# Optimization experiments

Hardware: AMD Instinct MI355X
Metric: run time of the kernel (lower is better)

The kernel has to match this reference:

```python
import jax, jax.numpy as jnp
import numpy as np

N_NODES = 50000
N_EDGES = 600000
N_GRAPHS = 512
DIM = 128
N_FEAT = 78
N_LAYERS = 4
BN_EPS = 1e-5


def setup_inputs() -> dict:
    key = jax.random.key(0)
    ks = jax.random.split(key, 12)
    w = lambda k, s: (jax.random.normal(k, s, jnp.float32) * 0.05)
    x = jax.random.normal(ks[0], (N_NODES, N_FEAT), jnp.float32)
    edge_index = jax.random.randint(ks[1], (2, N_EDGES), 0, N_NODES)
    batch = jnp.sort(jax.random.randint(ks[2], (N_NODES,), 0, N_GRAPHS))
    return {
        "x": x,
        "edge_index": edge_index,
        "batch": batch,
        "ini_w1": w(ks[3], (N_FEAT, DIM)),
        "ini_b1": jnp.zeros((DIM,), jnp.float32),
        "ini_w2": w(ks[4], (DIM, DIM)),
        "ini_b2": jnp.zeros((DIM,), jnp.float32),
        "gin_w1": w(ks[5], (N_LAYERS, DIM, DIM)),
        "gin_b1": jnp.zeros((N_LAYERS, DIM), jnp.float32),
        "gin_w2": w(ks[6], (N_LAYERS, DIM, DIM)),
        "gin_b2": jnp.zeros((N_LAYERS, DIM), jnp.float32),
        "bn_gamma": jnp.ones((N_LAYERS, DIM), jnp.float32),
        "bn_beta": jnp.zeros((N_LAYERS, DIM), jnp.float32),
        "layer_w": w(ks[7], (N_LAYERS,)),  # Conv2d(L,1,(1,1)) weight
        "layer_b": jnp.zeros((1,), jnp.float32),
    }


def reference(x, edge_index, batch, ini_w1, ini_b1, ini_w2, ini_b2,
              gin_w1, gin_b1, gin_w2, gin_b2, bn_gamma, bn_beta,
              layer_w, layer_b):
    # ini_embed: Linear -> ReLU -> Linear
    h = jnp.maximum(x @ ini_w1 + ini_b1, 0.0) @ ini_w2 + ini_b2  # [N, D]
    src, dst = edge_index[0], edge_index[1]
    embeds = []
    for i in range(N_LAYERS):
        # GINConv (eps=0): mlp(x_i + sum_{j->i} x_j)
        agg = jax.ops.segment_sum(h[src], dst, num_segments=N_NODES)
        z = h + agg
        z = jnp.maximum(z @ gin_w1[i] + gin_b1[i], 0.0) @ gin_w2[i] + gin_b2[i]
        z = jnp.maximum(z, 0.0)  # F.relu after conv
        # BatchNorm1d (training mode: batch stats, biased var)
        mean = jnp.mean(z, axis=0)
        var = jnp.mean((z - mean) ** 2, axis=0)
        h = (z - mean) * jax.lax.rsqrt(var + BN_EPS) * bn_gamma[i] + bn_beta[i]
        embeds.append(h)
    layer_nodes = jnp.stack(embeds, axis=1)  # [N, L, D]
    # layer_conv Conv2d(L,1,(1,1)): learned weighted sum over layer axis + bias
    pos_global_node = jnp.einsum('nld,l->nd', layer_nodes, layer_w) + layer_b
    # global_add_pool over graphs
    pos_global_graph = jax.ops.segment_sum(pos_global_node, batch,
                                           num_segments=N_GRAPHS)  # [G, D]
    return pos_global_graph
```

## Files before the change

kernel.cpp:

```cpp
#include <hip/hip_runtime.h>

#define N_NODES  50000
#define N_EDGES  600000
#define N_GRAPHS 512
#define DIM      128
#define N_FEAT   78
#define N_LAYERS 4
#define BN_EPS   1e-5f
#define SLOT_CAP 64
#define LDA      136
#define NPART    16

#define NBKT     196
#define NBLK_BIN 128
#define BCAP     64
#define EDGES_PER_BIN ((N_EDGES + NBLK_BIN - 1) / NBLK_BIN)

#define GSTART_BLOCKS 196
#define ZERO_BLOCKS 512
#define GBLOCKS ((N_NODES + 63) / 64)
#define TW_ELEMS (10 * 16384)
#define BN_FLOATS (N_LAYERS * NPART * 256)

typedef __attribute__((ext_vector_type(8))) _Float16 f16x8;
typedef __attribute__((ext_vector_type(4))) float f32x4;

static __device__ __forceinline__ short f2h(float f) {
    _Float16 h = (_Float16)f;
    union { _Float16 h; short s; } u; u.h = h;
    return u.s;
}
static __device__ __forceinline__ float h2f(ushort s) {
    union { ushort s; _Float16 h; } u; u.s = s;
    return (float)u.h;
}


__global__ __launch_bounds__(256) void transpose_weights(const float* __restrict__ ini_w1,
                                                         const float* __restrict__ ini_w2,
                                                         const float* __restrict__ gw1,
                                                         const float* __restrict__ gw2,
                                                         short* __restrict__ wt,
                                                         float* __restrict__ bnstat) {
    int gid = blockIdx.x * 256 + threadIdx.x;
    if (gid < TW_ELEMS) {
        int m = gid >> 14;
        int idx = gid & 16383;
        int n = idx >> 7;
        int k = idx & 127;
        const float* src;
        int K = 128;
        if (m == 0) { src = ini_w1; K = N_FEAT; }
        else if (m == 1) src = ini_w2;
        else if (m < 6) src = gw1 + (m - 2) * 16384;
        else src = gw2 + (m - 6) * 16384;
        float v = (k < K) ? src[k * 128 + n] : 0.f;
        wt[m * 16384 + n * 128 + k] = f2h(v);
    } else {
        int bi = gid - TW_ELEMS;
        if (bi < BN_FLOATS) bnstat[bi] = 0.0f;
    }
}


__global__ __launch_bounds__(256, 4) void ini_fused(const float* __restrict__ x,
                                                    const short* __restrict__ Wt1,
                                                    const float* __restrict__ b1,
                                                    const short* __restrict__ Wt2,
                                                    const float* __restrict__ b2,
                                                    ushort* __restrict__ Cout,
                                                    const int* __restrict__ src,
                                                    const int* __restrict__ dst,
                                                    const int* __restrict__ batch,
                                                    int* __restrict__ bcnt,
                                                    uint* __restrict__ bpool,
                                                    int* __restrict__ gstart,
                                                    float* __restrict__ gsum,
                                                    float* __restrict__ gssq) {
    __shared__ short As[64 * LDA];
    __shared__ short Bs[64 * LDA];
    int tid = threadIdx.x;

    if (blockIdx.x >= GBLOCKS) {
        int b = blockIdx.x - GBLOCKS;
        if (b < NBLK_BIN) {
            int* lcur = (int*)As;
            for (int i = tid; i < NBKT; i += 256) lcur[i] = 0;
            __syncthreads();
            int base = b * EDGES_PER_BIN;
            int lim = min(base + EDGES_PER_BIN, N_EDGES);
            for (int e = base + tid; e < lim; e += 256) {
                int d = dst[e];
                int s = src[e];
                int bk = d >> 8;
                int p = atomicAdd(&lcur[bk], 1);
                if (p < BCAP)
                    bpool[(bk * NBLK_BIN + b) * BCAP + p] =
                        ((uint)(d & 255) << 16) | (uint)s;
            }
            __syncthreads();
            for (int i = tid; i < NBKT; i += 256) bcnt[b * NBKT + i] = lcur[i];
            return;
        }
        b -= NBLK_BIN;
        if (b < GSTART_BLOCKS) {
            int n = b * 256 + tid;
            if (n < N_NODES) {
                int g = batch[n];
                int gp = (n == 0) ? -1 : batch[n - 1];
                for (int gg = gp + 1; gg <= g; ++gg) gstart[gg] = n;
                if (n == N_NODES - 1)
                    for (int gg = g + 1; gg <= N_GRAPHS; ++gg) gstart[gg] = N_NODES;
            }
            return;
        }
        b -= GSTART_BLOCKS;
        float4 z = make_float4(0.f, 0.f, 0.f, 0.f);
        float* bse = (b < 256) ? gsum : gssq;
        int off = (b & 255) * 1024 + tid * 4;
        *(float4*)&bse[off] = z;
        return;
    }

    int row0 = blockIdx.x * 64;
    int wave = tid >> 6;
    int wlane = tid & 63;
    int rw = wave >> 1;
    int cw = wave & 1;
    int lm = wlane & 15;
    int quad = wlane >> 4;
    const int wrow = (cw * 64 + lm) * 128 + quad * 8;

    f16x8 bcur[4], bnxt[4];
    #pragma unroll
    for (int nt = 0; nt < 4; ++nt)
        bcur[nt] = *(const f16x8*)&Wt1[wrow + nt * 2048];

    #pragma unroll
    for (int j = 0; j < 32; ++j) {
        int lin = tid + j * 256;
        int r = lin >> 7;
        int k = lin & 127;
        int gr = row0 + r;
        float v = 0.f;
        if (gr < N_NODES && k < N_FEAT) v = x[gr * N_FEAT + k];
        As[r * LDA + k] = f2h(v);
    }
    __syncthreads();

    f32x4 acc[2][4];
    #pragma unroll
    for (int mt = 0; mt < 2; ++mt)
        #pragma unroll
        for (int nt = 0; nt < 4; ++nt)
            acc[mt][nt] = (f32x4){0.f, 0.f, 0.f, 0.f};

    #pragma unroll
    for (int ks = 0; ks < 4; ++ks) {
        if (ks < 3) {
            #pragma unroll
            for (int nt = 0; nt < 4; ++nt)
                bnxt[nt] = *(const f16x8*)&Wt1[wrow + nt * 2048 + (ks + 1) * 32];
        }
        int kb = ks * 32 + quad * 8;
        f16x8 a0 = *(const f16x8*)&As[(rw * 32 + lm) * LDA + kb];
        f16x8 a1 = *(const f16x8*)&As[(rw * 32 + 16 + lm) * LDA + kb];
        #pragma unroll
        for (int nt = 0; nt < 4; ++nt) {
            acc[0][nt] = __builtin_amdgcn_mfma_f32_16x16x32_f16(a0, bcur[nt], acc[0][nt], 0, 0, 0);
            acc[1][nt] = __builtin_amdgcn_mfma_f32_16x16x32_f16(a1, bcur[nt], acc[1][nt], 0, 0, 0);
        }
        #pragma unroll
        for (int nt = 0; nt < 4; ++nt) bcur[nt] = bnxt[nt];
    }

    #pragma unroll
    for (int nt = 0; nt < 4; ++nt) {
        int col = cw * 64 + nt * 16 + lm;
        float bv = b1[col];
        #pragma unroll
        for (int mt = 0; mt < 2; ++mt) {
            #pragma unroll
            for (int r = 0; r < 4; ++r) {
                int row = rw * 32 + mt * 16 + quad * 4 + r;
                Bs[row * LDA + col] = (short)f2h(fmaxf(acc[mt][nt][r] + bv, 0.f));
            }
        }
    }
    #pragma unroll
    for (int nt = 0; nt < 4; ++nt)
        bcur[nt] = *(const f16x8*)&Wt2[wrow + nt * 2048];
    __syncthreads();

    #pragma unroll
    for (int mt = 0; mt < 2; ++mt)
        #pragma unroll
        for (int nt = 0; nt < 4; ++nt)
            acc[mt][nt] = (f32x4){0.f, 0.f, 0.f, 0.f};
    #pragma unroll
    for (int ks = 0; ks < 4; ++ks) {
        if (ks < 3) {
            #pragma unroll
            for (int nt = 0; nt < 4; ++nt)
                bnxt[nt] = *(const f16x8*)&Wt2[wrow + nt * 2048 + (ks + 1) * 32];
        }
        int kb = ks * 32 + quad * 8;
        f16x8 a0 = *(const f16x8*)&Bs[(rw * 32 + lm) * LDA + kb];
        f16x8 a1 = *(const f16x8*)&Bs[(rw * 32 + 16 + lm) * LDA + kb];
        #pragma unroll
        for (int nt = 0; nt < 4; ++nt) {
            acc[0][nt] = __builtin_amdgcn_mfma_f32_16x16x32_f16(a0, bcur[nt], acc[0][nt], 0, 0, 0);
            acc[1][nt] = __builtin_amdgcn_mfma_f32_16x16x32_f16(a1, bcur[nt], acc[1][nt], 0, 0, 0);
        }
        #pragma unroll
        for (int nt = 0; nt < 4; ++nt) bcur[nt] = bnxt[nt];
    }

    ushort* Cs = (ushort*)As;
    #pragma unroll
    for (int nt = 0; nt < 4; ++nt) {
        int col = cw * 64 + nt * 16 + lm;
        float bv = b2[col];
        #pragma unroll
        for (int mt = 0; mt < 2; ++mt) {
            #pragma unroll
            for (int r = 0; r < 4; ++r) {
                int row = rw * 32 + mt * 16 + quad * 4 + r;
                Cs[row * LDA + col] = (ushort)f2h(acc[mt][nt][r] + bv);
            }
        }
    }
    __syncthreads();

    #pragma unroll
    for (int j = 0; j < 4; ++j) {
        int lin = tid + j * 256;
        int r = lin >> 4;
        int kc = lin & 15;
        int gr = row0 + r;
        if (gr < N_NODES)
            *(uint4*)&Cout[gr * 128 + kc * 8] = *(const uint4*)&Cs[r * LDA + kc * 8];
    }
}


__global__ __launch_bounds__(256) void build_slot(const uint* __restrict__ bpool,
                                                  const int* __restrict__ bcnt,
                                                  int* __restrict__ cnt,
                                                  ushort* __restrict__ slot) {
    __shared__ ushort lslot[256 * SLOT_CAP];
    __shared__ int lcnt[256];
    __shared__ int rcnt[NBLK_BIN];
    int tid = threadIdx.x;
    int bkt = blockIdx.x;
    lcnt[tid] = 0;
    if (tid < NBLK_BIN) rcnt[tid] = min(bcnt[tid * NBKT + bkt], BCAP);
    __syncthreads();
    const uint* pool = bpool + (size_t)bkt * NBLK_BIN * BCAP;
    #pragma unroll 1
    for (int i = tid; i < NBLK_BIN * BCAP; i += 256) {
        int run = i >> 6;
        int pos = i & (BCAP - 1);
        if (pos < rcnt[run]) {
            uint u = pool[i];
            int ls = u >> 16;
            int p = atomicAdd(&lcnt[ls], 1);
            if (p < SLOT_CAP) lslot[ls * SLOT_CAP + p] = (ushort)(u & 0xffffu);
        }
    }
    __syncthreads();
    int node0 = bkt << 8;
    int gn = node0 + tid;
    if (gn < N_NODES) cnt[gn] = lcnt[tid];
    #pragma unroll
    for (int j = 0; j < 8; ++j) {
        int i = tid + j * 256;
        int r = i >> 3;
        int c = i & 7;
        int g = node0 + r;
        if (g < N_NODES)
            *(uint4*)&slot[g * SLOT_CAP + c * 8] = *(const uint4*)&lslot[r * SLOT_CAP + c * 8];
    }
}


__global__ __launch_bounds__(256) void aggregate_h(const ushort* __restrict__ Z,
                                                   const int* __restrict__ cnt,
                                                   const ushort* __restrict__ slot,
                                                   const float* __restrict__ bnpart,
                                                   const float* __restrict__ gamma,
                                                   const float* __restrict__ beta,
                                                   ushort* __restrict__ A) {
    __shared__ float saff[128], taff[128];
    int tid = threadIdx.x;
    if (tid < 128) {
        float s = 1.0f, t = 0.0f;
        if (bnpart) {
            float sum = 0.f, ssq = 0.f;
            #pragma unroll
            for (int p = 0; p < NPART; ++p) {
                sum += bnpart[p * 256 + tid];
                ssq += bnpart[p * 256 + 128 + tid];
            }
            const float invN = 1.0f / (float)N_NODES;
            float m = sum * invN;
            float var = ssq * invN - m * m;
            s = gamma[tid] * rsqrtf(var + BN_EPS);
            t = beta[tid] - m * s;
        }
        saff[tid] = s; taff[tid] = t;
    }
    __syncthreads();

    int node = blockIdx.x * 16 + (tid >> 4);
    if (node >= N_NODES) return;
    int lane = tid & 15;
    float sc[8], tc[8];
    #pragma unroll
    for (int j = 0; j < 8; ++j) {
        sc[j] = saff[lane * 8 + j];
        tc[j] = taff[lane * 8 + j];
    }
    union U { uint4 u; _Float16 h[8]; };
    union I { uint4 u; ushort s[8]; };
    const uint4* z4 = (const uint4*)Z;
    U zu; zu.u = z4[node * 16 + lane];
    float v[8];
    #pragma unroll
    for (int j = 0; j < 8; ++j) v[j] = (float)zu.h[j];
    int dtrue = cnt[node];
    int d = min(dtrue, SLOT_CAP);
    const ushort* sl = slot + node * SLOT_CAP;
    int e = 0;
    for (; e + 8 <= d; e += 8) {
        I si; si.u = *(const uint4*)&sl[e];
        U u[8];
        #pragma unroll
        for (int q = 0; q < 8; ++q) u[q].u = z4[(int)si.s[q] * 16 + lane];
        #pragma unroll
        for (int j = 0; j < 8; ++j) {
            float a = ((float)u[0].h[j] + (float)u[1].h[j]) +
                      ((float)u[2].h[j] + (float)u[3].h[j]);
            float b = ((float)u[4].h[j] + (float)u[5].h[j]) +
                      ((float)u[6].h[j] + (float)u[7].h[j]);
            v[j] += a + b;
        }
    }
    if (e + 4 <= d) {
        int s0 = sl[e], s1 = sl[e + 1], s2 = sl[e + 2], s3 = sl[e + 3];
        U u0, u1, u2, u3;
        u0.u = z4[s0 * 16 + lane];
        u1.u = z4[s1 * 16 + lane];
        u2.u = z4[s2 * 16 + lane];
        u3.u = z4[s3 * 16 + lane];
        #pragma unroll
        for (int j = 0; j < 8; ++j)
            v[j] += ((float)u0.h[j] + (float)u1.h[j]) +
                    ((float)u2.h[j] + (float)u3.h[j]);
        e += 4;
    }
    for (; e < d; ++e) {
        U u; u.u = z4[(int)sl[e] * 16 + lane];
        #pragma unroll
        for (int j = 0; j < 8; ++j) v[j] += (float)u.h[j];
    }
    float dsc = 1.0f + (float)dtrue;
    U ou;
    #pragma unroll
    for (int j = 0; j < 8; ++j)
        ou.h[j] = (_Float16)(sc[j] * v[j] + dsc * tc[j]);
    ((uint4*)A)[node * 16 + lane] = ou.u;
}


__global__ __launch_bounds__(256, 4) void gemm_gin(const ushort* __restrict__ A,
                                                   const short* __restrict__ Wt1,
                                                   const float* __restrict__ b1,
                                                   const short* __restrict__ Wt2,
                                                   const float* __restrict__ b2,
                                                   ushort* __restrict__ C,
                                                   const int* __restrict__ batch,
                                                   float* __restrict__ gsum,
                                                   float* __restrict__ gssq,
                                                   float* __restrict__ bnpart) {
    __shared__ short Bs[64 * LDA];
    __shared__ float scr[256];
    __shared__ int sb[64];
    int tid = threadIdx.x;
    int row0 = blockIdx.x * 64;

    int wave = tid >> 6;
    int wlane = tid & 63;
    int rw = wave >> 1;
    int cw = wave & 1;
    int lm = wlane & 15;
    int quad = wlane >> 4;
    const int wrow = (cw * 64 + lm) * 128 + quad * 8;

    if (tid < 64) {
        int n = row0 + tid;
        sb[tid] = (n < N_NODES) ? batch[n] : -1;
    }

    int r0 = min(row0 + rw * 32 + lm, N_NODES - 1);
    int r1 = min(row0 + rw * 32 + 16 + lm, N_NODES - 1);
    const ushort* arow0 = A + r0 * 128 + quad * 8;
    const ushort* arow1 = A + r1 * 128 + quad * 8;

    f16x8 bcur[4], bnxt[4];
    #pragma unroll
    for (int nt = 0; nt < 4; ++nt)
        bcur[nt] = *(const f16x8*)&Wt1[wrow + nt * 2048];

    f32x4 acc[2][4];
    #pragma unroll
    for (int mt = 0; mt < 2; ++mt)
        #pragma unroll
        for (int nt = 0; nt < 4; ++nt)
            acc[mt][nt] = (f32x4){0.f, 0.f, 0.f, 0.f};

    f16x8 a0 = *(const f16x8*)arow0;
    f16x8 a1 = *(const f16x8*)arow1;
    #pragma unroll
    for (int ks = 0; ks < 4; ++ks) {
        f16x8 a0n, a1n;
        if (ks < 3) {
            a0n = *(const f16x8*)(arow0 + (ks + 1) * 32);
            a1n = *(const f16x8*)(arow1 + (ks + 1) * 32);
            #pragma unroll
            for (int nt = 0; nt < 4; ++nt)
                bnxt[nt] = *(const f16x8*)&Wt1[wrow + nt * 2048 + (ks + 1) * 32];
        }
        #pragma unroll
        for (int nt = 0; nt < 4; ++nt) {
            acc[0][nt] = __builtin_amdgcn_mfma_f32_16x16x32_f16(a0, bcur[nt], acc[0][nt], 0, 0, 0);
            acc[1][nt] = __builtin_amdgcn_mfma_f32_16x16x32_f16(a1, bcur[nt], acc[1][nt], 0, 0, 0);
        }
        a0 = a0n; a1 = a1n;
        #pragma unroll
        for (int nt = 0; nt < 4; ++nt) bcur[nt] = bnxt[nt];
    }

    #pragma unroll
    for (int nt = 0; nt < 4; ++nt) {
        int col = cw * 64 + nt * 16 + lm;
        float bv = b1[col];
        #pragma unroll
        for (int mt = 0; mt < 2; ++mt) {
            #pragma unroll
            for (int r = 0; r < 4; ++r) {
                int row = rw * 32 + mt * 16 + quad * 4 + r;
                Bs[row * LDA + col] = (short)f2h(fmaxf(acc[mt][nt][r] + bv, 0.f));
            }
        }
    }
    #pragma unroll
    for (int nt = 0; nt < 4; ++nt)
        bcur[nt] = *(const f16x8*)&Wt2[wrow + nt * 2048];
    __syncthreads();

    #pragma unroll
    for (int mt = 0; mt < 2; ++mt)
        #pragma unroll
        for (int nt = 0; nt < 4; ++nt)
            acc[mt][nt] = (f32x4){0.f, 0.f, 0.f, 0.f};
    #pragma unroll
    for (int ks = 0; ks < 4; ++ks) {
        if (ks < 3) {
            #pragma unroll
            for (int nt = 0; nt < 4; ++nt)
                bnxt[nt] = *(const f16x8*)&Wt2[wrow + nt * 2048 + (ks + 1) * 32];
        }
        int kb = ks * 32 + quad * 8;
        f16x8 c0 = *(const f16x8*)&Bs[(rw * 32 + lm) * LDA + kb];
        f16x8 c1 = *(const f16x8*)&Bs[(rw * 32 + 16 + lm) * LDA + kb];
        #pragma unroll
        for (int nt = 0; nt < 4; ++nt) {
            acc[0][nt] = __builtin_amdgcn_mfma_f32_16x16x32_f16(c0, bcur[nt], acc[0][nt], 0, 0, 0);
            acc[1][nt] = __builtin_amdgcn_mfma_f32_16x16x32_f16(c1, bcur[nt], acc[1][nt], 0, 0, 0);
        }
        #pragma unroll
        for (int nt = 0; nt < 4; ++nt) bcur[nt] = bnxt[nt];
    }
    __syncthreads();

    ushort* Cs = (ushort*)Bs;
    #pragma unroll
    for (int nt = 0; nt < 4; ++nt) {
        int col = cw * 64 + nt * 16 + lm;
        float bv = b2[col];
        #pragma unroll
        for (int mt = 0; mt < 2; ++mt) {
            #pragma unroll
            for (int r = 0; r < 4; ++r) {
                int row = rw * 32 + mt * 16 + quad * 4 + r;
                Cs[row * LDA + col] = (ushort)f2h(fmaxf(acc[mt][nt][r] + bv, 0.f));
            }
        }
    }
    __syncthreads();

    #pragma unroll
    for (int j = 0; j < 4; ++j) {
        int lin = tid + j * 256;
        int r = lin >> 4;
        int kc = lin & 15;
        int gr = row0 + r;
        if (gr < N_NODES)
            *(uint4*)&C[gr * 128 + kc * 8] = *(const uint4*)&Cs[r * LDA + kc * 8];
    }

    {
        int c = tid & 127;
        int rbase = (tid >> 7) * 32;
        int curg = sb[rbase];
        float rs = 0.f, rss = 0.f;
        float ts = 0.f, tss = 0.f;
        for (int r = rbase; r < rbase + 32; ++r) {
            int g = sb[r];
            if (g < 0) break;
            if (g != curg) {
                atomicAdd(&gsum[curg * 128 + c], rs);
                atomicAdd(&gssq[curg * 128 + c], rss);
                rs = 0.f; rss = 0.f; curg = g;
            }
            float v = h2f(Cs[r * LDA + c]);
            rs += v; rss += v * v;
            ts += v; tss += v * v;
        }
        if (curg >= 0) {
            atomicAdd(&gsum[curg * 128 + c], rs);
            atomicAdd(&gssq[curg * 128 + c], rss);
        }
        if (tid >= 128) { scr[c] = ts; scr[128 + c] = tss; }
        __syncthreads();
        if (tid < 128) {
            float* part = bnpart + (blockIdx.x & (NPART - 1)) * 256;
            atomicAdd(&part[c], ts + scr[c]);
            atomicAdd(&part[128 + c], tss + scr[128 + c]);
        }
    }
}


__global__ __launch_bounds__(256) void combine(const float* __restrict__ gsum,
                                               const float* __restrict__ bnstat,
                                               const int* __restrict__ gstart,
                                               const float* __restrict__ gamma,
                                               const float* __restrict__ beta,
                                               const float* __restrict__ LW,
                                               const float* __restrict__ LB,
                                               float* __restrict__ out) {
    int gid = blockIdx.x * 256 + threadIdx.x;
    if (gid >= N_GRAPHS * 128) return;
    int g = gid >> 7;
    int d = gid & 127;
    float c = (float)(gstart[g + 1] - gstart[g]);
    float o = c * LB[0];
    const float invN = 1.0f / (float)N_NODES;
    #pragma unroll
    for (int l = 0; l < N_LAYERS; ++l) {
        const float* part = bnstat + l * NPART * 256;
        float sum = 0.f, ssq = 0.f;
        #pragma unroll
        for (int p = 0; p < NPART; ++p) {
            sum += part[p * 256 + d];
            ssq += part[p * 256 + 128 + d];
        }
        float m = sum * invN;
        float var = ssq * invN - m * m;
        float s = gamma[l * 128 + d] * rsqrtf(var + BN_EPS);
        float t = beta[l * 128 + d] - m * s;
        o += LW[l] * (s * gsum[(l * N_GRAPHS + g) * 128 + d] + c * t);
    }
    out[gid] = o;
}


extern "C" void kernel_launch(void* const* d_in, const int* in_sizes, int n_in,
                              void* d_out, int out_size, void* d_ws, size_t ws_size,
                              hipStream_t stream) {
    const float* x      = (const float*)d_in[0];
    const int*   ei     = (const int*)d_in[1];
    const int*   batch  = (const int*)d_in[2];
    const float* ini_w1 = (const float*)d_in[3];
    const float* ini_b1 = (const float*)d_in[4];
    const float* ini_w2 = (const float*)d_in[5];
    const float* ini_b2 = (const float*)d_in[6];
    const float* gw1    = (const float*)d_in[7];
    const float* gb1    = (const float*)d_in[8];
    const float* gw2    = (const float*)d_in[9];
    const float* gb2    = (const float*)d_in[10];
    const float* gamma  = (const float*)d_in[11];
    const float* beta   = (const float*)d_in[12];
    const float* lw     = (const float*)d_in[13];
    const float* lb     = (const float*)d_in[14];
    float* out = (float*)d_out;

    char* p = (char*)d_ws;
    auto carve = [&](size_t bytes) -> char* {
        char* q = p;
        p += (bytes + 255) & ~(size_t)255;
        return q;
    };
    ushort* z0    = (ushort*)carve(sizeof(ushort) * N_NODES * DIM);
    ushort* z1    = (ushort*)carve(sizeof(ushort) * N_NODES * DIM);
    ushort* abuf  = (ushort*)carve(sizeof(ushort) * N_NODES * DIM);
    float* bnstat = (float*)carve(sizeof(float) * BN_FLOATS);
    float* gsum   = (float*)carve(sizeof(float) * N_LAYERS * N_GRAPHS * DIM);
    float* gssq   = (float*)carve(sizeof(float) * N_LAYERS * N_GRAPHS * DIM);
    short* wbf    = (short*)carve(sizeof(short) * 10 * 128 * 128);
    int* gstart   = (int*)carve(sizeof(int) * (N_GRAPHS + 1));
    int* cnt      = (int*)carve(sizeof(int) * N_NODES);
    ushort* slot  = (ushort*)carve(sizeof(ushort) * N_NODES * SLOT_CAP);
    int* bcnt     = (int*)carve(sizeof(int) * NBLK_BIN * NBKT);
    uint* bpool   = (uint*)abuf;

    const int* src = ei;
    const int* dst = ei + N_EDGES;

    int twblocks = (TW_ELEMS + BN_FLOATS + 255) / 256;
    transpose_weights<<<twblocks, 256, 0, stream>>>(
        ini_w1, ini_w2, gw1, gw2, wbf, bnstat);

    ini_fused<<<GBLOCKS + NBLK_BIN + GSTART_BLOCKS + ZERO_BLOCKS, 256, 0, stream>>>(
        x, wbf, ini_b1, wbf + 16384, ini_b2, z0,
        src, dst, batch, bcnt, bpool, gstart, gsum, gssq);

    build_slot<<<NBKT, 256, 0, stream>>>(bpool, bcnt, cnt, slot);

    ushort* zprev = z0;
    ushort* znext = z1;
    for (int i = 0; i < N_LAYERS; ++i) {
        const float* bp_in = (i == 0) ? nullptr : bnstat + (i - 1) * NPART * 256;
        const float* gptr  = (i == 0) ? gamma : gamma + (i - 1) * DIM;
        const float* bptr  = (i == 0) ? beta : beta + (i - 1) * DIM;
        aggregate_h<<<(N_NODES + 15) / 16, 256, 0, stream>>>(
            zprev, cnt, slot, bp_in, gptr, bptr, abuf);
        gemm_gin<<<GBLOCKS, 256, 0, stream>>>(
            abuf, wbf + (2 + i) * 16384, gb1 + i * DIM,
            wbf + (6 + i) * 16384, gb2 + i * DIM, znext, batch,
            gsum + i * N_GRAPHS * DIM, gssq + i * N_GRAPHS * DIM,
            bnstat + i * NPART * 256);
        ushort* tmp = zprev; zprev = znext; znext = tmp;
    }
    combine<<<(N_GRAPHS * 128 + 255) / 256, 256, 0, stream>>>(
        gsum, bnstat, gstart, gamma, beta, lw, lb, out);
}
```

Baseline: 354.5 us.

## Fuse neighbor aggregation into GIN GEMM kernel via shared-memory A tile

```diff
diff --git a/kernel.cpp b/kernel.cpp
--- a/kernel.cpp
+++ b/kernel.cpp
@@ -284,106 +284,24 @@
 }
 
 
-__global__ __launch_bounds__(256) void aggregate_h(const ushort* __restrict__ Z,
-                                                   const int* __restrict__ cnt,
-                                                   const ushort* __restrict__ slot,
-                                                   const float* __restrict__ bnpart,
-                                                   const float* __restrict__ gamma,
-                                                   const float* __restrict__ beta,
-                                                   ushort* __restrict__ A) {
+__global__ __launch_bounds__(256, 4) void gin_fused(const ushort* __restrict__ Z,
+                                                    const int* __restrict__ cnt,
+                                                    const ushort* __restrict__ slot,
+                                                    const float* __restrict__ bnpart,
+                                                    const float* __restrict__ gamma,
+                                                    const float* __restrict__ beta,
+                                                    const short* __restrict__ Wt1,
+                                                    const float* __restrict__ b1,
+                                                    const short* __restrict__ Wt2,
+                                                    const float* __restrict__ b2,
+                                                    ushort* __restrict__ C,
+                                                    const int* __restrict__ batch,
+                                                    float* __restrict__ gsum,
+                                                    float* __restrict__ gssq,
+                                                    float* __restrict__ bnpart_out) {
+    __shared__ short As[64 * LDA];
+    __shared__ short Bs[64 * LDA];
     __shared__ float saff[128], taff[128];
-    int tid = threadIdx.x;
-    if (tid < 128) {
-        float s = 1.0f, t = 0.0f;
-        if (bnpart) {
-            float sum = 0.f, ssq = 0.f;
-            #pragma unroll
-            for (int p = 0; p < NPART; ++p) {
-                sum += bnpart[p * 256 + tid];
-                ssq += bnpart[p * 256 + 128 + tid];
-            }
-            const float invN = 1.0f / (float)N_NODES;
-            float m = sum * invN;
-            float var = ssq * invN - m * m;
-            s = gamma[tid] * rsqrtf(var + BN_EPS);
-            t = beta[tid] - m * s;
-        }
-        saff[tid] = s; taff[tid] = t;
-    }
-    __syncthreads();
-
-    int node = blockIdx.x * 16 + (tid >> 4);
-    if (node >= N_NODES) return;
-    int lane = tid & 15;
-    float sc[8], tc[8];
-    #pragma unroll
-    for (int j = 0; j < 8; ++j) {
-        sc[j] = saff[lane * 8 + j];
-        tc[j] = taff[lane * 8 + j];
-    }
-    union U { uint4 u; _Float16 h[8]; };
-    union I { uint4 u; ushort s[8]; };
-    const uint4* z4 = (const uint4*)Z;
-    U zu; zu.u = z4[node * 16 + lane];
-    float v[8];
-    #pragma unroll
-    for (int j = 0; j < 8; ++j) v[j] = (float)zu.h[j];
-    int dtrue = cnt[node];
-    int d = min(dtrue, SLOT_CAP);
-    const ushort* sl = slot + node * SLOT_CAP;
-    int e = 0;
-    for (; e + 8 <= d; e += 8) {
-        I si; si.u = *(const uint4*)&sl[e];
-        U u[8];
-        #pragma unroll
-        for (int q = 0; q < 8; ++q) u[q].u = z4[(int)si.s[q] * 16 + lane];
-        #pragma unroll
-        for (int j = 0; j < 8; ++j) {
-            float a = ((float)u[0].h[j] + (float)u[1].h[j]) +
-                      ((float)u[2].h[j] + (float)u[3].h[j]);
-            float b = ((float)u[4].h[j] + (float)u[5].h[j]) +
-                      ((float)u[6].h[j] + (float)u[7].h[j]);
-            v[j] += a + b;
-        }
-    }
-    if (e + 4 <= d) {
-        int s0 = sl[e], s1 = sl[e + 1], s2 = sl[e + 2], s3 = sl[e + 3];
-        U u0, u1, u2, u3;
-        u0.u = z4[s0 * 16 + lane];
-        u1.u = z4[s1 * 16 + lane];
-        u2.u = z4[s2 * 16 + lane];
-        u3.u = z4[s3 * 16 + lane];
-        #pragma unroll
-        for (int j = 0; j < 8; ++j)
-            v[j] += ((float)u0.h[j] + (float)u1.h[j]) +
-                    ((float)u2.h[j] + (float)u3.h[j]);
-        e += 4;
-    }
-    for (; e < d; ++e) {
-        U u; u.u = z4[(int)sl[e] * 16 + lane];
-        #pragma unroll
-        for (int j = 0; j < 8; ++j) v[j] += (float)u.h[j];
-    }
-    float dsc = 1.0f + (float)dtrue;
-    U ou;
-    #pragma unroll
-    for (int j = 0; j < 8; ++j)
-        ou.h[j] = (_Float16)(sc[j] * v[j] + dsc * tc[j]);
-    ((uint4*)A)[node * 16 + lane] = ou.u;
-}
-
-
-__global__ __launch_bounds__(256, 4) void gemm_gin(const ushort* __restrict__ A,
-                                                   const short* __restrict__ Wt1,
-                                                   const float* __restrict__ b1,
-                                                   const short* __restrict__ Wt2,
-                                                   const float* __restrict__ b2,
-                                                   ushort* __restrict__ C,
-                                                   const int* __restrict__ batch,
-                                                   float* __restrict__ gsum,
-                                                   float* __restrict__ gssq,
-                                                   float* __restrict__ bnpart) {
-    __shared__ short Bs[64 * LDA];
     __shared__ float scr[256];
     __shared__ int sb[64];
     int tid = threadIdx.x;
@@ -397,20 +315,100 @@
     int quad = wlane >> 4;
     const int wrow = (cw * 64 + lm) * 128 + quad * 8;
 
+    if (tid < 128) {
+        float s = 1.0f, t = 0.0f;
+        if (bnpart) {
+            float sum = 0.f, ssq = 0.f;
+            #pragma unroll
+            for (int p = 0; p < NPART; ++p) {
+                sum += bnpart[p * 256 + tid];
+                ssq += bnpart[p * 256 + 128 + tid];
+            }
+            const float invN = 1.0f / (float)N_NODES;
+            float m = sum * invN;
+            float var = ssq * invN - m * m;
+            s = gamma[tid] * rsqrtf(var + BN_EPS);
+            t = beta[tid] - m * s;
+        }
+        saff[tid] = s; taff[tid] = t;
+    }
     if (tid < 64) {
         int n = row0 + tid;
         sb[tid] = (n < N_NODES) ? batch[n] : -1;
     }
-
-    int r0 = min(row0 + rw * 32 + lm, N_NODES - 1);
-    int r1 = min(row0 + rw * 32 + 16 + lm, N_NODES - 1);
-    const ushort* arow0 = A + r0 * 128 + quad * 8;
-    const ushort* arow1 = A + r1 * 128 + quad * 8;
+    __syncthreads();
+
+    {
+        int lane = tid & 15;
+        int nsub = tid >> 4;
+        union U { uint4 u; _Float16 h[8]; };
+        union I { uint4 u; ushort s[8]; };
+        const uint4* z4 = (const uint4*)Z;
+        #pragma unroll 1
+        for (int pass = 0; pass < 4; ++pass) {
+            int r = pass * 16 + nsub;
+            int node = row0 + r;
+            float v[8];
+            float dsc = 1.0f;
+            if (node < N_NODES) {
+                U zu; zu.u = z4[node * 16 + lane];
+                #pragma unroll
+                for (int j = 0; j < 8; ++j) v[j] = (float)zu.h[j];
+                int dtrue = cnt[node];
+                int d = min(dtrue, SLOT_CAP);
+                const ushort* sl = slot + node * SLOT_CAP;
+                int e = 0;
+                for (; e + 8 <= d; e += 8) {
+                    I si; si.u = *(const uint4*)&sl[e];
+                    U u[8];
+                    #pragma unroll
+                    for (int q = 0; q < 8; ++q) u[q].u = z4[(int)si.s[q] * 16 + lane];
+                    #pragma unroll
+                    for (int j = 0; j < 8; ++j) {
+                        float a = ((float)u[0].h[j] + (float)u[1].h[j]) +
+                                  ((float)u[2].h[j] + (float)u[3].h[j]);
+                        float b = ((float)u[4].h[j] + (float)u[5].h[j]) +
+                                  ((float)u[6].h[j] + (float)u[7].h[j]);
+                        v[j] += a + b;
+                    }
+                }
+                if (e + 4 <= d) {
+                    int s0 = sl[e], s1 = sl[e + 1], s2 = sl[e + 2], s3 = sl[e + 3];
+                    U u0, u1, u2, u3;
+                    u0.u = z4[s0 * 16 + lane];
+                    u1.u = z4[s1 * 16 + lane];
+                    u2.u = z4[s2 * 16 + lane];
+                    u3.u = z4[s3 * 16 + lane];
+                    #pragma unroll
+                    for (int j = 0; j < 8; ++j)
+                        v[j] += ((float)u0.h[j] + (float)u1.h[j]) +
+                                ((float)u2.h[j] + (float)u3.h[j]);
+                    e += 4;
+                }
+                for (; e < d; ++e) {
+                    U u; u.u = z4[(int)sl[e] * 16 + lane];
+                    #pragma unroll
+                    for (int j = 0; j < 8; ++j) v[j] += (float)u.h[j];
+                }
+                dsc = 1.0f + (float)dtrue;
+            } else {
+                #pragma unroll
+                for (int j = 0; j < 8; ++j) v[j] = 0.f;
+                dsc = 0.f;
+            }
+            #pragma unroll
+            for (int j = 0; j < 8; ++j) {
+                int dd = lane * 8 + j;
+                As[r * LDA + dd] = f2h(saff[dd] * v[j] + dsc * taff[dd]);
+            }
+        }
+    }
 
     f16x8 bcur[4], bnxt[4];
     #pragma unroll
     for (int nt = 0; nt < 4; ++nt)
         bcur[nt] = *(const f16x8*)&Wt1[wrow + nt * 2048];
+    __syncthreads();
 
     f32x4 acc[2][4];
     #pragma unroll
@@ -418,29 +416,24 @@
         #pragma unroll
         for (int nt = 0; nt < 4; ++nt)
             acc[mt][nt] = (f32x4){0.f, 0.f, 0.f, 0.f};
-
-    f16x8 a0 = *(const f16x8*)arow0;
-    f16x8 a1 = *(const f16x8*)arow1;
     #pragma unroll
     for (int ks = 0; ks < 4; ++ks) {
-        f16x8 a0n, a1n;
         if (ks < 3) {
-            a0n = *(const f16x8*)(arow0 + (ks + 1) * 32);
-            a1n = *(const f16x8*)(arow1 + (ks + 1) * 32);
             #pragma unroll
             for (int nt = 0; nt < 4; ++nt)
                 bnxt[nt] = *(const f16x8*)&Wt1[wrow + nt * 2048 + (ks + 1) * 32];
         }
+        int kb = ks * 32 + quad * 8;
+        f16x8 a0 = *(const f16x8*)&As[(rw * 32 + lm) * LDA + kb];
+        f16x8 a1 = *(const f16x8*)&As[(rw * 32 + 16 + lm) * LDA + kb];
         #pragma unroll
         for (int nt = 0; nt < 4; ++nt) {
             acc[0][nt] = __builtin_amdgcn_mfma_f32_16x16x32_f16(a0, bcur[nt], acc[0][nt], 0, 0, 0);
             acc[1][nt] = __builtin_amdgcn_mfma_f32_16x16x32_f16(a1, bcur[nt], acc[1][nt], 0, 0, 0);
         }
-        a0 = a0n; a1 = a1n;
         #pragma unroll
         for (int nt = 0; nt < 4; ++nt) bcur[nt] = bnxt[nt];
     }
-
     #pragma unroll
     for (int nt = 0; nt < 4; ++nt) {
         int col = cw * 64 + nt * 16 + lm;
@@ -482,9 +475,7 @@
         #pragma unroll
         for (int nt = 0; nt < 4; ++nt) bcur[nt] = bnxt[nt];
     }
-    __syncthreads();
-
-    ushort* Cs = (ushort*)Bs;
+    ushort* Cs = (ushort*)As;
     #pragma unroll
     for (int nt = 0; nt < 4; ++nt) {
         int col = cw * 64 + nt * 16 + lm;
@@ -535,7 +526,7 @@
         if (tid >= 128) { scr[c] = ts; scr[128 + c] = tss; }
         __syncthreads();
         if (tid < 128) {
-            float* part = bnpart + (blockIdx.x & (NPART - 1)) * 256;
+            float* part = bnpart_out + (blockIdx.x & (NPART - 1)) * 256;
             atomicAdd(&part[c], ts + scr[c]);
             atomicAdd(&part[128 + c], tss + scr[128 + c]);
         }
@@ -605,7 +596,6 @@
     };
     ushort* z0    = (ushort*)carve(sizeof(ushort) * N_NODES * DIM);
     ushort* z1    = (ushort*)carve(sizeof(ushort) * N_NODES * DIM);
-    ushort* abuf  = (ushort*)carve(sizeof(ushort) * N_NODES * DIM);
     float* bnstat = (float*)carve(sizeof(float) * BN_FLOATS);
     float* gsum   = (float*)carve(sizeof(float) * N_LAYERS * N_GRAPHS * DIM);
     float* gssq   = (float*)carve(sizeof(float) * N_LAYERS * N_GRAPHS * DIM);
@@ -614,7 +604,7 @@
     int* cnt      = (int*)carve(sizeof(int) * N_NODES);
     ushort* slot  = (ushort*)carve(sizeof(ushort) * N_NODES * SLOT_CAP);
     int* bcnt     = (int*)carve(sizeof(int) * NBLK_BIN * NBKT);
-    uint* bpool   = (uint*)abuf;
+    uint* bpool   = (uint*)carve(sizeof(uint) * NBKT * NBLK_BIN * BCAP);
 
     const int* src = ei;
     const int* dst = ei + N_EDGES;
@@ -635,10 +625,9 @@
         const float* bp_in = (i == 0) ? nullptr : bnstat + (i - 1) * NPART * 256;
         const float* gptr  = (i == 0) ? gamma : gamma + (i - 1) * DIM;
         const float* bptr  = (i == 0) ? beta : beta + (i - 1) * DIM;
-        aggregate_h<<<(N_NODES + 15) / 16, 256, 0, stream>>>(
-            zprev, cnt, slot, bp_in, gptr, bptr, abuf);
-        gemm_gin<<<GBLOCKS, 256, 0, stream>>>(
-            abuf, wbf + (2 + i) * 16384, gb1 + i * DIM,
+        gin_fused<<<GBLOCKS, 256, 0, stream>>>(
+            zprev, cnt, slot, bp_in, gptr, bptr,
+            wbf + (2 + i) * 16384, gb1 + i * DIM,
             wbf + (6 + i) * 16384, gb2 + i * DIM, znext, batch,
             gsum + i * N_GRAPHS * DIM, gssq + i * N_GRAPHS * DIM,
             bnstat + i * NPART * 256);
```

New measurement: 317.6 us. -10.4%, faster.
